# Kernel optimization log

Measured on AMD Instinct MI355X. Metric: run time of the kernel, lower is better.

Reference implementation:

```python
import jax, jax.numpy as jnp
import numpy as np
from jax import lax
import math

POOL = 7
SPATIAL_SCALE = 0.125
SCORE_THRESH = 0.05
NMS_THRESH = 0.5
DET_PER_IMG = 100
NUM_CLASSES = 81
NUM_STAGES = 3
FEAT_CH = 256
CLIP_VAL = math.log(1000.0 / 16)
STDS = ((0.1, 0.1, 0.2, 0.2), (0.05, 0.05, 0.1, 0.1), (0.033, 0.033, 0.067, 0.067))


def setup_inputs() -> dict:
    key = jax.random.key(0)
    ks = jax.random.split(key, 12)
    B, N, img = 2, 512, 512
    features = jax.random.normal(ks[0], (B, FEAT_CH, 64, 64), jnp.float32)
    cx = jax.random.uniform(ks[1], (B, N)) * img
    cy = jax.random.uniform(ks[2], (B, N)) * img
    w = 16.0 + jax.random.uniform(ks[3], (B, N)) * 240.0
    h = 16.0 + jax.random.uniform(ks[4], (B, N)) * 240.0
    proposals = jnp.stack([
        jnp.clip(cx - 0.5 * w, 0.0, img), jnp.clip(cy - 0.5 * h, 0.0, img),
        jnp.clip(cx + 0.5 * w, 0.0, img), jnp.clip(cy + 0.5 * h, 0.0, img)], axis=-1)
    in_dim = FEAT_CH * POOL * POOL
    sc = 0.02
    return {
        'features': features,
        'proposals': proposals,
        'fc1_w': jax.random.normal(ks[5], (NUM_STAGES, in_dim, 1024), jnp.float32) * sc,
        'fc1_b': jnp.zeros((NUM_STAGES, 1024), jnp.float32),
        'fc2_w': jax.random.normal(ks[6], (NUM_STAGES, 1024, 1024), jnp.float32) * sc,
        'fc2_b': jnp.zeros((NUM_STAGES, 1024), jnp.float32),
        'cls_w': jax.random.normal(ks[7], (NUM_STAGES, 1024, NUM_CLASSES), jnp.float32) * sc,
        'cls_b': jnp.zeros((NUM_STAGES, NUM_CLASSES), jnp.float32),
        'bbox_w': jax.random.normal(ks[8], (NUM_STAGES, 1024, 4), jnp.float32) * sc,
        'bbox_b': jnp.zeros((NUM_STAGES, 4), jnp.float32),
        'image_size': 512,
    }


def _bilinear(feat, gx, gy):
    # feat [C,H,W]; gx,gy [N,P,P] float coords
    C, H, W = feat.shape
    x = jnp.clip(gx, 0.0, W - 1.0)
    y = jnp.clip(gy, 0.0, H - 1.0)
    x0f, y0f = jnp.floor(x), jnp.floor(y)
    x0 = x0f.astype(jnp.int32)
    y0 = y0f.astype(jnp.int32)
    x1 = jnp.minimum(x0 + 1, W - 1)
    y1 = jnp.minimum(y0 + 1, H - 1)
    dx = (x - x0f)[None]
    dy = (y - y0f)[None]
    v = (feat[:, y0, x0] * (1 - dy) * (1 - dx) + feat[:, y0, x1] * (1 - dy) * dx
         + feat[:, y1, x0] * dy * (1 - dx) + feat[:, y1, x1] * dy * dx)
    return v  # [C,N,P,P]


def roi_align(feat, boxes):
    # feat [C,H,W], boxes [N,4] in feature-map coords
    x1, y1, x2, y2 = boxes[:, 0], boxes[:, 1], boxes[:, 2], boxes[:, 3]
    bw = jnp.maximum(x2 - x1, 1.0) / POOL
    bh = jnp.maximum(y2 - y1, 1.0) / POOL
    c = jnp.arange(POOL, dtype=boxes.dtype) + 0.5
    xs = x1[:, None] + c * bw[:, None]  # [N,P]
    ys = y1[:, None] + c * bh[:, None]
    N = boxes.shape[0]
    gx = jnp.broadcast_to(xs[:, None, :], (N, POOL, POOL))
    gy = jnp.broadcast_to(ys[:, :, None], (N, POOL, POOL))
    return jnp.transpose(_bilinear(feat, gx, gy), (1, 0, 2, 3))  # [N,C,P,P]


def decode_boxes(proposals, deltas, stds):
    px1, py1, px2, py2 = proposals[:, 0], proposals[:, 1], proposals[:, 2], proposals[:, 3]
    pw = jnp.maximum(px2 - px1, 1e-6)
    ph = jnp.maximum(py2 - py1, 1e-6)
    pcx = px1 + 0.5 * pw
    pcy = py1 + 0.5 * ph
    wx, wy, ww, wh = stds
    dx = deltas[:, 0] * wx
    dy = deltas[:, 1] * wy
    dw = jnp.minimum(deltas[:, 2] * ww, CLIP_VAL)
    dh = jnp.minimum(deltas[:, 3] * wh, CLIP_VAL)
    cx = dx * pw + pcx
    cy = dy * ph + pcy
    w = jnp.exp(dw) * pw
    h = jnp.exp(dh) * ph
    return jnp.stack([cx - 0.5 * w, cy - 0.5 * h, cx + 0.5 * w, cy + 0.5 * h], axis=1)


def clip_boxes(b, img):
    return jnp.stack([jnp.clip(b[:, 0], 0.0, img), jnp.clip(b[:, 1], 0.0, img),
                      jnp.clip(b[:, 2], 0.0, img), jnp.clip(b[:, 3], 0.0, img)], axis=1)


def nms_per_image(boxes, probs, img):
    # boxes [N,4], probs [N,C]
    N, C = probs.shape
    Cm = C - 1  # skip background class 0
    labels = jnp.broadcast_to(jnp.arange(1, C, dtype=jnp.int32), (N, Cm)).reshape(-1)
    b = jnp.broadcast_to(boxes[:, None, :], (N, Cm, 4)).reshape(-1, 4)
    s = probs[:, 1:].reshape(-1)
    ws = b[:, 2] - b[:, 0]
    hs = b[:, 3] - b[:, 1]
    valid = (s > SCORE_THRESH) & (ws >= 1.0) & (hs >= 1.0)
    s = jnp.where(valid, s, -1.0)
    # class-offset trick == batched_nms
    ob = b + (labels.astype(b.dtype) * (img + 2.0))[:, None]
    area = jnp.maximum(ob[:, 2] - ob[:, 0], 0.0) * jnp.maximum(ob[:, 3] - ob[:, 1], 0.0)

    def step(s_live, _):
        i = jnp.argmax(s_live)
        si = s_live[i]
        bi = ob[i]
        ix1 = jnp.maximum(bi[0], ob[:, 0])
        iy1 = jnp.maximum(bi[1], ob[:, 1])
        ix2 = jnp.minimum(bi[2], ob[:, 2])
        iy2 = jnp.minimum(bi[3], ob[:, 3])
        inter = jnp.maximum(ix2 - ix1, 0.0) * jnp.maximum(iy2 - iy1, 0.0)
        iou = inter / (area[i] + area - inter + 1e-9)
        s_live = jnp.where(iou > NMS_THRESH, -1.0, s_live)
        s_live = s_live.at[i].set(-1.0)
        return s_live, (i, si)

    _, (idx, sel_s) = lax.scan(step, s, None, length=DET_PER_IMG)
    flag = sel_s > 0.0
    out_boxes = jnp.where(flag[:, None], b[idx], 0.0)
    out_scores = jnp.where(flag, sel_s, 0.0)
    out_labels = jnp.where(flag, labels[idx], 0)
    return out_boxes, out_scores, out_labels


def reference(features, proposals, fc1_w, fc1_b, fc2_w, fc2_b, cls_w, cls_b, bbox_w, bbox_b, image_size):
    B, Cf, H, W = features.shape
    N = proposals.shape[1]
    img = float(image_size)
    cur = proposals  # [B,N,4]
    logits = None
    for st in range(NUM_STAGES):
        pooled = jax.vmap(lambda f, bx: roi_align(f, bx * SPATIAL_SCALE))(features, cur)  # [B,N,C,P,P]
        x = pooled.reshape(B * N, -1)
        x = jax.nn.relu(x @ fc1_w[st] + fc1_b[st])
        x = jax.nn.relu(x @ fc2_w[st] + fc2_b[st])
        logits = x @ cls_w[st] + cls_b[st]  # [B*N, C]
        deltas = x @ bbox_w[st] + bbox_b[st]  # [B*N, 4]
        dec = clip_boxes(decode_boxes(cur.reshape(-1, 4), deltas, STDS[st]), img)
        cur = dec.reshape(B, N, 4)
    probs = jax.nn.softmax(logits.reshape(B, N, -1), axis=-1)
    boxes, scores, labels = jax.vmap(lambda bb, pp: nms_per_image(bb, pp, img))(cur, probs)
    return boxes, scores, labels
```

## Files before the change

kernel.cpp:

```cpp
#include <hip/hip_runtime.h>
#include <math.h>

#define NPROP 512
#define NB 2
#define NROWS (NB*NPROP)
#define FCH 256
#define FH 64
#define FW 64
#define INDIM (FCH*7*7)
#define HID 1024
#define NCLS 81
#define CAND_PER_IMG (NPROP*(NCLS-1))
#define CLIPV 4.1351666f

typedef _Float16 f16x8 __attribute__((ext_vector_type(8)));
typedef float f32x4 __attribute__((ext_vector_type(4)));
typedef unsigned int u32;
typedef unsigned long long u64;

__device__ __forceinline__ void gload16(const void* g, void* l) {
    __builtin_amdgcn_global_load_lds((const __attribute__((address_space(1))) u32*)g,
                                     (__attribute__((address_space(3))) u32*)l, 16, 0, 0);
}

#define XHI_OFF    0ull
#define XLO_OFF    25690112ull
#define WT1HI_OFF  51380224ull
#define WT1LO_OFF  77070336ull
#define WT2HI_OFF  102760448ull
#define WT2LO_OFF  104857600ull
#define H1HI_OFF   106954752ull
#define H1LO_OFF   109051904ull
#define H2_OFF     111149056ull
#define CWT_OFF    115343360ull
#define BWT_OFF    116338688ull
#define PROBS_OFF  116387840ull
#define CUR_OFF    116719616ull
#define CNT_OFF    116736000ull
#define CCS_OFF    116737024ull
#define CCOB_OFF   117064704ull
#define CCAR_OFF   118375424ull
#define CCBX_OFF   118703104ull
#define CCIX_OFF   120013824ull
#define SVS_OFF    120341504ull
#define SVB_OFF    120423424ull
#define SVI_OFF    120751104ull
#define SVC_OFF    120833024ull
#define PART_OFF   121489408ull

__global__ void init_kernel(int* ccnt) {
    if (threadIdx.x < 160) ccnt[threadIdx.x] = 0;
}

__global__ __launch_bounds__(256) void roi_align_kernel(
    const float* __restrict__ feat, const float* __restrict__ boxes,
    _Float16* __restrict__ Xhi, _Float16* __restrict__ Xlo)
{
    int r = blockIdx.x;
    int b = r >> 9;
    const float* f = feat + (size_t)b * (FCH*FH*FW);
    __shared__ float sb[4];
    __shared__ int   sx0[49], sx1[49], sy0[49], sy1[49];
    __shared__ float sw00[49], sw01[49], sw10[49], sw11[49];
    int tid = threadIdx.x;
    if (tid == 0) {
        float x1 = boxes[r*4+0]*0.125f, y1 = boxes[r*4+1]*0.125f;
        float x2 = boxes[r*4+2]*0.125f, y2 = boxes[r*4+3]*0.125f;
        sb[0] = x1; sb[1] = y1;
        sb[2] = fmaxf(x2-x1, 1.0f) / 7.0f;
        sb[3] = fmaxf(y2-y1, 1.0f) / 7.0f;
    }
    __syncthreads();
    if (tid < 49) {
        int py = tid / 7, px = tid - py*7;
        float gx = sb[0] + ((float)px + 0.5f)*sb[2];
        float gy = sb[1] + ((float)py + 0.5f)*sb[3];
        gx = fminf(fmaxf(gx, 0.0f), 63.0f);
        gy = fminf(fmaxf(gy, 0.0f), 63.0f);
        float x0f = floorf(gx), y0f = floorf(gy);
        int x0 = (int)x0f, y0 = (int)y0f;
        sx0[tid] = x0; sy0[tid] = y0;
        sx1[tid] = min(x0+1, 63); sy1[tid] = min(y0+1, 63);
        float dx = gx - x0f, dy = gy - y0f;
        sw00[tid] = (1.0f-dy)*(1.0f-dx);
        sw01[tid] = (1.0f-dy)*dx;
        sw10[tid] = dy*(1.0f-dx);
        sw11[tid] = dy*dx;
    }
    __syncthreads();
    size_t xbase = (size_t)r * INDIM;
    for (int i = tid; i < INDIM; i += 256) {
        int c = i / 49;
        int p = i - c*49;
        const float* fc = f + c*(FH*FW);
        int r0 = sy0[p]*FW, r1 = sy1[p]*FW;
        float v = fc[r0 + sx0[p]]*sw00[p] + fc[r0 + sx1[p]]*sw01[p]
                + fc[r1 + sx0[p]]*sw10[p] + fc[r1 + sx1[p]]*sw11[p];
        float vs = v * 32.0f;
        _Float16 h = (_Float16)vs;
        Xhi[xbase + i] = h;
        Xlo[xbase + i] = (_Float16)(vs - (float)h);
    }
}

__global__ __launch_bounds__(256) void trans_limb(
    const float* __restrict__ in, _Float16* __restrict__ hi, _Float16* __restrict__ lo,
    int K, int N, float scale)
{
    __shared__ float t[32][33];
    int tx = threadIdx.x & 31, ty = threadIdx.x >> 5;
    int n0 = blockIdx.x << 5, k0 = blockIdx.y << 5;
#pragma unroll
    for (int r = 0; r < 4; ++r)
        t[ty + 8*r][tx] = in[(size_t)(k0 + ty + 8*r)*N + n0 + tx];
    __syncthreads();
#pragma unroll
    for (int r = 0; r < 4; ++r) {
        int n = n0 + ty + 8*r, k = k0 + tx;
        float v = t[tx][ty + 8*r] * scale;
        _Float16 h = (_Float16)v;
        hi[(size_t)n*K + k] = h;
        lo[(size_t)n*K + k] = (_Float16)(v - (float)h);
    }
}

__global__ __launch_bounds__(256) void trans_naive(
    const float* __restrict__ in, float* __restrict__ out, int K, int N, int batch)
{
    int idx = blockIdx.x*256 + threadIdx.x;
    int per = K*N;
    if (idx >= per*batch) return;
    int b = idx / per;
    int rem = idx - b*per;
    int n = rem / K, k = rem - n*K;
    out[idx] = in[(size_t)b*per + (size_t)k*N + n];
}

__global__ __launch_bounds__(512, 2) void mfma_gemm_limb256(
    const _Float16* __restrict__ Ahi, const _Float16* __restrict__ Alo,
    const _Float16* __restrict__ Bhi, const _Float16* __restrict__ Blo,
    float* __restrict__ part, int K, int base, int extra)
{
    extern __shared__ __align__(16) char ldsraw[];
    const int tid = threadIdx.x;
    const int lane = tid & 63;
    const int w = tid >> 6;
    const int wm = w >> 2, wn = w & 3;
    const int kg = lane >> 4, lr = lane & 15;
    const int bid = blockIdx.x;
    const int z = bid & 15;
    const int tile = bid >> 4;
    const int bx = tile & 3, by = tile >> 2;
    const int row0 = by << 8, col0 = bx << 8;
    const int zsteps = base + (z < extra ? 1 : 0);
    const int kb0 = (z*base + (z < extra ? z : extra)) * 32;

    const int sp = w >> 1;
    const int sbase = (w & 1) * 8;
    const _Float16* pl = (sp == 0) ? Ahi : (sp == 1) ? Alo : (sp == 2) ? Bhi : Blo;
    const int rc0 = (sp < 2) ? row0 : col0;
    const _Float16* sG = pl + (size_t)(rc0 + lane)*K + kb0;

    f32x4 acc[8][4];
#pragma unroll
    for (int i = 0; i < 8; ++i)
#pragma unroll
        for (int j = 0; j < 4; ++j) acc[i][j] = (f32x4){0.f, 0.f, 0.f, 0.f};

    auto STAGE = [&](int bufoff, int koff) {
#pragma unroll
        for (int j = 0; j < 8; ++j) {
            int sub = sbase + j;
            int ks = sub >> 2, rblk = sub & 3;
            const void* g = (const void*)(sG + (size_t)(rblk*64)*K + koff + ks*8);
            void* l = (void*)(ldsraw + bufoff + sp*16384 + ks*4096 + rblk*1024);
            gload16(g, l);
        }
    };

    STAGE(0, 0);
    if (zsteps > 1) STAGE(65536, 32);

    for (int t = 0; t < zsteps; ++t) {
        if (t + 1 < zsteps) asm volatile("s_waitcnt vmcnt(8)" ::: "memory");
        else                asm volatile("s_waitcnt vmcnt(0)" ::: "memory");
        __builtin_amdgcn_s_barrier();
        asm volatile("" ::: "memory");
        const char* Lb = ldsraw + ((t & 1) ? 65536 : 0);
        f16x8 Bh[4], Bl[4];
#pragma unroll
        for (int ni = 0; ni < 4; ++ni) {
            int s = (kg*256 + wn*64 + ni*16 + lr) * 16;
            Bh[ni] = *(const f16x8*)(Lb + 2*16384 + s);
            Bl[ni] = *(const f16x8*)(Lb + 3*16384 + s);
        }
#pragma unroll
        for (int mi = 0; mi < 8; ++mi) {
            int s = (kg*256 + wm*128 + mi*16 + lr) * 16;
            f16x8 ah = *(const f16x8*)(Lb + s);
            f16x8 al = *(const f16x8*)(Lb + 16384 + s);
#pragma unroll
            for (int ni = 0; ni < 4; ++ni) {
                acc[mi][ni] = __builtin_amdgcn_mfma_f32_16x16x32_f16(ah, Bh[ni], acc[mi][ni], 0, 0, 0);
                acc[mi][ni] = __builtin_amdgcn_mfma_f32_16x16x32_f16(ah, Bl[ni], acc[mi][ni], 0, 0, 0);
                acc[mi][ni] = __builtin_amdgcn_mfma_f32_16x16x32_f16(al, Bh[ni], acc[mi][ni], 0, 0, 0);
            }
        }
        asm volatile("" ::: "memory");
        __builtin_amdgcn_s_barrier();
        asm volatile("" ::: "memory");
        if (t + 2 < zsteps) STAGE((t & 1) ? 65536 : 0, (t+2)*32);
    }

    float* cb = part + ((size_t)z << 20)
              + (size_t)row0*HID + col0 + wn*64 + lr;
#pragma unroll
    for (int mi = 0; mi < 8; ++mi) {
#pragma unroll
        for (int j = 0; j < 4; ++j) {
            int row = wm*128 + mi*16 + kg*4 + j;
            float* pr = cb + (size_t)row*HID;
            pr[0]  = acc[mi][0][j];
            pr[16] = acc[mi][1][j];
            pr[32] = acc[mi][2][j];
            pr[48] = acc[mi][3][j];
        }
    }
}

__global__ __launch_bounds__(256) void mfma_gemm_limb(
    const _Float16* __restrict__ Ahi, const _Float16* __restrict__ Alo,
    const _Float16* __restrict__ Bhi, const _Float16* __restrict__ Blo,
    float* __restrict__ part, int K, int base, int extra, int lognz)
{
    __shared__ __align__(16) _Float16 lds[2][4][512][8];
    const int tid = threadIdx.x;
    const int lane = tid & 63;
    const int w = tid >> 6, wm = w >> 1, wn = w & 1;
    const int kg = lane >> 4, lr = lane & 15;
    const int bid = blockIdx.x;
    const int nzm = (1 << lognz) - 1;
    const int z = bid & nzm;
    const int bx = (bid >> lognz) & 7;
    const int by = bid >> (lognz + 3);
    const int row0 = by << 7, col0 = bx << 7;
    const int zsteps = base + (z < extra ? 1 : 0);
    const int kb0 = (z*base + (z < extra ? z : extra)) * 32;
    const int r_ = tid & 127;
    const int ks1 = tid >> 7;
    const int wb = tid & 192;

    const _Float16* srcA0 = Ahi + (size_t)(row0 + r_) * K + kb0 + ks1*8;
    const _Float16* srcA1 = Alo + (size_t)(row0 + r_) * K + kb0 + ks1*8;
    const _Float16* srcB0 = Bhi + (size_t)(col0 + r_) * K + kb0 + ks1*8;
    const _Float16* srcB1 = Blo + (size_t)(col0 + r_) * K + kb0 + ks1*8;

    f32x4 acc[4][4];
#pragma unroll
    for (int i = 0; i < 4; ++i)
#pragma unroll
        for (int j = 0; j < 4; ++j) acc[i][j] = (f32x4){0.f, 0.f, 0.f, 0.f};

#define STAGE(bf, off) do { \
    _Float16* Lb = &lds[bf][0][0][0]; \
    gload16(srcA0 + (off),      (void*)(Lb + (0*512 +       wb)*8)); \
    gload16(srcA0 + (off) + 16, (void*)(Lb + (0*512 + 256 + wb)*8)); \
    gload16(srcA1 + (off),      (void*)(Lb + (1*512 +       wb)*8)); \
    gload16(srcA1 + (off) + 16, (void*)(Lb + (1*512 + 256 + wb)*8)); \
    gload16(srcB0 + (off),      (void*)(Lb + (2*512 +       wb)*8)); \
    gload16(srcB0 + (off) + 16, (void*)(Lb + (2*512 + 256 + wb)*8)); \
    gload16(srcB1 + (off),      (void*)(Lb + (3*512 +       wb)*8)); \
    gload16(srcB1 + (off) + 16, (void*)(Lb + (3*512 + 256 + wb)*8)); \
} while (0)

    STAGE(0, 0);
    if (1 < zsteps) STAGE(1, 32);
    for (int t = 0; t < zsteps; ++t) {
        if (t + 1 < zsteps) asm volatile("s_waitcnt vmcnt(8)" ::: "memory");
        else                asm volatile("s_waitcnt vmcnt(0)" ::: "memory");
        __builtin_amdgcn_s_barrier();
        const _Float16* Lr = &lds[t & 1][0][0][0];
        f16x8 Ah[4], Al[4], Bh[4], Bl[4];
#pragma unroll
        for (int mi = 0; mi < 4; ++mi) {
            int s = kg*128 + wm*64 + mi*16 + lr;
            Ah[mi] = *(const f16x8*)(Lr + (0*512 + s)*8);
            Al[mi] = *(const f16x8*)(Lr + (1*512 + s)*8);
        }
#pragma unroll
        for (int ni = 0; ni < 4; ++ni) {
            int s = kg*128 + wn*64 + ni*16 + lr;
            Bh[ni] = *(const f16x8*)(Lr + (2*512 + s)*8);
            Bl[ni] = *(const f16x8*)(Lr + (3*512 + s)*8);
        }
        asm volatile("s_waitcnt lgkmcnt(0)" ::: "memory");
        __builtin_amdgcn_sched_barrier(0);
        __builtin_amdgcn_s_barrier();
        if (t + 2 < zsteps) STAGE(t & 1, (t+2)*32);
#pragma unroll
        for (int mi = 0; mi < 4; ++mi)
#pragma unroll
            for (int ni = 0; ni < 4; ++ni) {
                acc[mi][ni] = __builtin_amdgcn_mfma_f32_16x16x32_f16(Ah[mi], Bh[ni], acc[mi][ni], 0, 0, 0);
                acc[mi][ni] = __builtin_amdgcn_mfma_f32_16x16x32_f16(Ah[mi], Bl[ni], acc[mi][ni], 0, 0, 0);
                acc[mi][ni] = __builtin_amdgcn_mfma_f32_16x16x32_f16(Al[mi], Bh[ni], acc[mi][ni], 0, 0, 0);
            }
    }
#undef STAGE

    float* cb = part + ((size_t)z << 20)
              + (size_t)row0*HID + col0 + wn*64 + lr;
#pragma unroll
    for (int mi = 0; mi < 4; ++mi) {
#pragma unroll
        for (int j = 0; j < 4; ++j) {
            int row = wm*64 + mi*16 + kg*4 + j;
            float* pr = cb + (size_t)row*HID;
            pr[0]  = acc[mi][0][j];
            pr[16] = acc[mi][1][j];
            pr[32] = acc[mi][2][j];
            pr[48] = acc[mi][3][j];
        }
    }
}

__global__ __launch_bounds__(256) void reduce_bias_relu(
    const float* __restrict__ part, const float* __restrict__ bias,
    float* __restrict__ out32, _Float16* __restrict__ outhi, _Float16* __restrict__ outlo,
    int nsplit, int mode)
{
    int gid = blockIdx.x*256 + threadIdx.x;
    float s = 0.f;
    for (int p = 0; p < nsplit; ++p) s += part[((size_t)p << 20) + gid];
    s = s * (1.0f/2048.0f) + bias[gid & (HID-1)];
    s = fmaxf(s, 0.f);
    if (mode == 0) {
        out32[gid] = s;
    } else {
        float vs = s * 32.0f;
        _Float16 h = (_Float16)vs;
        outhi[gid] = h;
        outlo[gid] = (_Float16)(vs - (float)h);
    }
}

__global__ __launch_bounds__(512) void heads_kernel(
    const float* __restrict__ X, const float* __restrict__ cwT, const float* __restrict__ cb,
    const float* __restrict__ bwT, const float* __restrict__ bbb,
    float* __restrict__ cur, float* __restrict__ probs,
    const int* __restrict__ img_sz, int stage, int write_probs)
{
    __shared__ float xs[4][1024];
    __shared__ float lg[4][96];
    int tid = threadIdx.x;
    int lr = tid >> 7;
    int j  = tid & 127;
    int row0 = blockIdx.x * 4;
    for (int i = tid; i < 4096; i += 512)
        xs[i >> 10][i & 1023] = X[(size_t)(row0 + (i >> 10))*1024 + (i & 1023)];
    __syncthreads();
    int row = row0 + lr;
    if (j < 85) {
        const float* wrow = (j < 81) ? (cwT + (size_t)j*HID) : (bwT + (size_t)(j-81)*HID);
        float acc = (j < 81) ? cb[j] : bbb[j-81];
        const float4* w4 = (const float4*)wrow;
#pragma unroll 4
        for (int k4 = 0; k4 < 256; ++k4) {
            float4 wv = w4[k4];
            const float* xr = &xs[lr][k4*4];
            acc = fmaf(xr[0], wv.x, acc);
            acc = fmaf(xr[1], wv.y, acc);
            acc = fmaf(xr[2], wv.z, acc);
            acc = fmaf(xr[3], wv.w, acc);
        }
        lg[lr][j] = acc;
    }
    __syncthreads();
    if (j == 0) {
        float img = (float)(*img_sz);
        float px1 = cur[row*4+0], py1 = cur[row*4+1];
        float px2 = cur[row*4+2], py2 = cur[row*4+3];
        float pw = fmaxf(px2-px1, 1e-6f), ph = fmaxf(py2-py1, 1e-6f);
        float pcx = px1 + 0.5f*pw, pcy = py1 + 0.5f*ph;
        float wx, wy, ww, wh;
        if (stage == 0)      { wx=0.1f;   wy=0.1f;   ww=0.2f;   wh=0.2f;   }
        else if (stage == 1) { wx=0.05f;  wy=0.05f;  ww=0.1f;   wh=0.1f;   }
        else                 { wx=0.033f; wy=0.033f; ww=0.067f; wh=0.067f; }
        float dx = lg[lr][81]*wx, dy = lg[lr][82]*wy;
        float dw = fminf(lg[lr][83]*ww, CLIPV);
        float dh = fminf(lg[lr][84]*wh, CLIPV);
        float cx = dx*pw + pcx, cy = dy*ph + pcy;
        float w = expf(dw)*pw, h = expf(dh)*ph;
        cur[row*4+0] = fminf(fmaxf(cx - 0.5f*w, 0.f), img);
        cur[row*4+1] = fminf(fmaxf(cy - 0.5f*h, 0.f), img);
        cur[row*4+2] = fminf(fmaxf(cx + 0.5f*w, 0.f), img);
        cur[row*4+3] = fminf(fmaxf(cy + 0.5f*h, 0.f), img);
    }
    if (write_probs) {
        if (j == 1) {
            float m = lg[lr][0];
            for (int c2 = 1; c2 < 81; ++c2) m = fmaxf(m, lg[lr][c2]);
            float s = 0.f;
            for (int c2 = 0; c2 < 81; ++c2) s += expf(lg[lr][c2] - m);
            lg[lr][88] = m; lg[lr][89] = s;
        }
        __syncthreads();
        if (j < 81)
            probs[(size_t)row*81 + j] = expf(lg[lr][j] - lg[lr][88]) / lg[lr][89];
    }
}

__global__ __launch_bounds__(256) void compact_class(
    const float* __restrict__ probs, const float* __restrict__ cur,
    const int* __restrict__ img_sz, int* __restrict__ ccnt,
    float* __restrict__ ccs, float4* __restrict__ ccob, float* __restrict__ ccar,
    float4* __restrict__ ccbx, int* __restrict__ ccix)
{
    int gid = blockIdx.x*256 + threadIdx.x;
    if (gid >= NB*CAND_PER_IMG) return;
    int b = gid / CAND_PER_IMG;
    int rem = gid - b*CAND_PER_IMG;
    int n = rem / 80;
    int cm = rem - n*80;
    int label = cm + 1;
    int r = b*NPROP + n;
    float s = probs[(size_t)r*81 + label];
    float b0 = cur[r*4+0], b1 = cur[r*4+1], b2 = cur[r*4+2], b3 = cur[r*4+3];
    if (s > 0.05f && (b2 - b0) >= 1.0f && (b3 - b1) >= 1.0f) {
        int cls = b*80 + cm;
        int pos = atomicAdd(&ccnt[cls], 1);
        int base = cls*512 + pos;
        float img = (float)(*img_sz);
        float t = (float)label * (img + 2.0f);
        float o0 = b0+t, o1 = b1+t, o2 = b2+t, o3 = b3+t;
        ccs[base] = s;
        ccob[base] = make_float4(o0, o1, o2, o3);
        ccar[base] = fmaxf(o2-o0, 0.f) * fmaxf(o3-o1, 0.f);
        ccbx[base] = make_float4(b0, b1, b2, b3);
        ccix[base] = rem;
    }
}

__global__ __launch_bounds__(64) void class_nms(
    const int* __restrict__ ccnt, const float* __restrict__ ccs,
    const float4* __restrict__ ccob, const float* __restrict__ ccar,
    const float4* __restrict__ ccbx, const int* __restrict__ ccix,
    float* __restrict__ svs, float4* __restrict__ svb, int* __restrict__ svi,
    int* __restrict__ svc)
{
    int cls = blockIdx.x;
    int Nc = ccnt[cls];
    int base = cls*512;
    int lane = threadIdx.x;
    __shared__ float sel[5];
    float s[8]; float4 ob[8]; float a[8]; int ix[8];
    int cntl = 0;
    for (int j = lane; j < Nc; j += 64) {
        s[cntl] = ccs[base+j]; ob[cntl] = ccob[base+j];
        a[cntl] = ccar[base+j]; ix[cntl] = ccix[base+j];
        ++cntl;
    }
    int svn = 0;
    int rounds = (Nc < 100) ? Nc : 100;
    for (int it = 0; it < rounds; ++it) {
        float bs = -1.f; int bi = 0x7fffffff;
        for (int q = 0; q < cntl; ++q)
            if (s[q] > bs || (s[q] == bs && ix[q] < bi)) { bs = s[q]; bi = ix[q]; }
        for (int off = 32; off > 0; off >>= 1) {
            float os = __shfl_xor(bs, off);
            int oi = __shfl_xor(bi, off);
            if (os > bs || (os == bs && oi < bi)) { bs = os; bi = oi; }
        }
        if (bs <= 0.f) break;
        for (int q = 0; q < cntl; ++q) {
            if (s[q] == bs && ix[q] == bi) {
                sel[0] = ob[q].x; sel[1] = ob[q].y; sel[2] = ob[q].z; sel[3] = ob[q].w;
                sel[4] = a[q];
                int slot = cls*128 + svn;
                svs[slot] = bs;
                svb[slot] = ccbx[base + lane + q*64];
                svi[slot] = bi;
                s[q] = -1.f;
            }
        }
        __syncthreads();
        float bi0 = sel[0], bi1 = sel[1], bi2 = sel[2], bi3 = sel[3], ai = sel[4];
        for (int q = 0; q < cntl; ++q) {
            if (s[q] > 0.f) {
                float ix1 = fmaxf(bi0, ob[q].x), iy1 = fmaxf(bi1, ob[q].y);
                float ix2 = fminf(bi2, ob[q].z), iy2 = fminf(bi3, ob[q].w);
                float inter = fmaxf(ix2-ix1, 0.f) * fmaxf(iy2-iy1, 0.f);
                float iou = inter / (ai + a[q] - inter + 1e-9f);
                if (iou > 0.5f) s[q] = -1.f;
            }
        }
        ++svn;
        __syncthreads();
    }
    if (lane == 0) svc[cls] = svn;
}

__global__ __launch_bounds__(256) void merge_topk(
    const float* __restrict__ svs, const float4* __restrict__ svb,
    const int* __restrict__ svi, const int* __restrict__ svc,
    float* __restrict__ out)
{
    extern __shared__ char smem[];
    u64* keys = (u64*)smem;
    u32* pay  = (u32*)(smem + 65536);
    __shared__ int off[81];
    __shared__ int n2s;
    int b = blockIdx.x, tid = threadIdx.x;
    if (tid == 0) {
        int run = 0;
        for (int c = 0; c < 80; ++c) { off[c] = run; run += svc[b*80 + c]; }
        off[80] = run;
        int n2 = 256;
        while (n2 < run) n2 <<= 1;
        n2s = n2;
    }
    __syncthreads();
    int Ns = off[80], n2 = n2s;
    for (int c = 0; c < 80; ++c) {
        int n = off[c+1] - off[c];
        int srcb = (b*80 + c)*128;
        for (int k = tid; k < n; k += 256) {
            int src = srcb + k;
            keys[off[c] + k] = ((u64)__float_as_uint(svs[src]) << 32)
                             | (u64)(0xFFFFFFFFu - (u32)svi[src]);
            pay[off[c] + k] = src;
        }
    }
    for (int i = Ns + tid; i < n2; i += 256) { keys[i] = 0; pay[i] = 0; }
    __syncthreads();
    for (int k = 2; k <= n2; k <<= 1) {
        for (int j = k >> 1; j > 0; j >>= 1) {
            for (int i = tid; i < n2; i += 256) {
                int l = i ^ j;
                if (l > i) {
                    u64 a = keys[i], bb = keys[l];
                    bool dir = ((i & k) == 0);
                    if ((a < bb) == dir) {
                        keys[i] = bb; keys[l] = a;
                        u32 p = pay[i]; pay[i] = pay[l]; pay[l] = p;
                    }
                }
            }
            __syncthreads();
        }
    }
    if (tid < 100) {
        u64 kk = keys[tid];
        if (kk != 0) {
            u32 ci = 0xFFFFFFFFu - (u32)(kk & 0xFFFFFFFFull);
            float4 bx = svb[pay[tid]];
            out[b*400 + tid*4 + 0] = bx.x;
            out[b*400 + tid*4 + 1] = bx.y;
            out[b*400 + tid*4 + 2] = bx.z;
            out[b*400 + tid*4 + 3] = bx.w;
            out[800  + b*100 + tid] = __uint_as_float((u32)(kk >> 32));
            out[1000 + b*100 + tid] = (float)((ci % 80) + 1);
        } else {
            out[b*400 + tid*4 + 0] = 0.f; out[b*400 + tid*4 + 1] = 0.f;
            out[b*400 + tid*4 + 2] = 0.f; out[b*400 + tid*4 + 3] = 0.f;
            out[800  + b*100 + tid] = 0.f;
            out[1000 + b*100 + tid] = 0.f;
        }
    }
}

extern "C" void kernel_launch(void* const* d_in, const int* in_sizes, int n_in,
                              void* d_out, int out_size, void* d_ws, size_t ws_size,
                              hipStream_t stream)
{
    const float* features  = (const float*)d_in[0];
    const float* proposals = (const float*)d_in[1];
    const float* fc1_w = (const float*)d_in[2];
    const float* fc1_b = (const float*)d_in[3];
    const float* fc2_w = (const float*)d_in[4];
    const float* fc2_b = (const float*)d_in[5];
    const float* cls_w = (const float*)d_in[6];
    const float* cls_b = (const float*)d_in[7];
    const float* bbox_w = (const float*)d_in[8];
    const float* bbox_b = (const float*)d_in[9];
    const int* img_sz = (const int*)d_in[10];
    float* out = (float*)d_out;
    char* ws = (char*)d_ws;
    _Float16* xhi   = (_Float16*)(ws + XHI_OFF);
    _Float16* xlo   = (_Float16*)(ws + XLO_OFF);
    _Float16* wt1hi = (_Float16*)(ws + WT1HI_OFF);
    _Float16* wt1lo = (_Float16*)(ws + WT1LO_OFF);
    _Float16* wt2hi = (_Float16*)(ws + WT2HI_OFF);
    _Float16* wt2lo = (_Float16*)(ws + WT2LO_OFF);
    _Float16* h1hi  = (_Float16*)(ws + H1HI_OFF);
    _Float16* h1lo  = (_Float16*)(ws + H1LO_OFF);
    float*  h2     = (float*) (ws + H2_OFF);
    float*  cwT    = (float*) (ws + CWT_OFF);
    float*  bwT    = (float*) (ws + BWT_OFF);
    float*  probs  = (float*) (ws + PROBS_OFF);
    float*  cur    = (float*) (ws + CUR_OFF);
    int*    ccnt   = (int*)   (ws + CNT_OFF);
    float*  ccs    = (float*) (ws + CCS_OFF);
    float4* ccob   = (float4*)(ws + CCOB_OFF);
    float*  ccar   = (float*) (ws + CCAR_OFF);
    float4* ccbx   = (float4*)(ws + CCBX_OFF);
    int*    ccix   = (int*)   (ws + CCIX_OFF);
    float*  svs    = (float*) (ws + SVS_OFF);
    float4* svb    = (float4*)(ws + SVB_OFF);
    int*    svi    = (int*)   (ws + SVI_OFF);
    int*    svc    = (int*)   (ws + SVC_OFF);
    float*  part   = (float*) (ws + PART_OFF);

    init_kernel<<<1, 256, 0, stream>>>(ccnt);
    hipMemcpyAsync(cur, proposals, (size_t)NROWS*4*sizeof(float),
                   hipMemcpyDeviceToDevice, stream);
    trans_naive<<<(3*NCLS*HID + 255)/256, 256, 0, stream>>>(cls_w, cwT, HID, NCLS, 3);
    trans_naive<<<(3*4*HID + 255)/256, 256, 0, stream>>>(bbox_w, bwT, HID, 4, 3);

    for (int st = 0; st < 3; ++st) {
        roi_align_kernel<<<NROWS, 256, 0, stream>>>(features, cur, xhi, xlo);
        trans_limb<<<dim3(HID/32, INDIM/32), 256, 0, stream>>>(
            fc1_w + (size_t)st*INDIM*HID, wt1hi, wt1lo, INDIM, HID, 64.0f);
        mfma_gemm_limb256<<<256, 512, 131072, stream>>>(
            xhi, xlo, wt1hi, wt1lo, part, INDIM, 24, 8);
        reduce_bias_relu<<<(NROWS*HID)/256, 256, 0, stream>>>(
            part, fc1_b + st*HID, nullptr, h1hi, h1lo, 16, 1);
        trans_limb<<<dim3(HID/32, HID/32), 256, 0, stream>>>(
            fc2_w + (size_t)st*HID*HID, wt2hi, wt2lo, HID, HID, 64.0f);
        mfma_gemm_limb<<<512, 256, 0, stream>>>(
            h1hi, h1lo, wt2hi, wt2lo, part, HID, 4, 0, 3);
        reduce_bias_relu<<<(NROWS*HID)/256, 256, 0, stream>>>(
            part, fc2_b + st*HID, h2, nullptr, nullptr, 8, 0);
        heads_kernel<<<NROWS/4, 512, 0, stream>>>(
            h2, cwT + (size_t)st*NCLS*HID, cls_b + st*NCLS,
            bwT + (size_t)st*4*HID, bbox_b + st*4,
            cur, probs, img_sz, st, st == 2 ? 1 : 0);
    }
    compact_class<<<(NB*CAND_PER_IMG)/256, 256, 0, stream>>>(
        probs, cur, img_sz, ccnt, ccs, ccob, ccar, ccbx, ccix);
    class_nms<<<160, 64, 0, stream>>>(
        ccnt, ccs, ccob, ccar, ccbx, ccix, svs, svb, svi, svc);
    merge_topk<<<NB, 256, 98304, stream>>>(
        svs, svb, svi, svc, out);
}
```

Before: 775.3 us.

## Store GEMM operands in k-octet-major layout for contiguous LDS staging loads

Changes the fp16 hi/lo operand buffers (ROI features, transposed weights, hidden activations) from row-major [rows][K] to an [K/8][rows][8] layout, so each 16-byte global_load_lds chunk for consecutive rows is contiguous. The GEMM kernels drop the K stride and index by k-octet. The goal is coalesced wide loads instead of loads strided by K per lane. The producers' writes now scatter in 16-byte pieces, which may cost store efficiency in roi_align, trans_limb and reduce.

```diff
diff --git a/kernel.cpp b/kernel.cpp
--- a/kernel.cpp
+++ b/kernel.cpp
@@ -22,6 +22,7 @@
     __builtin_amdgcn_global_load_lds((const __attribute__((address_space(1))) u32*)g,
                                      (__attribute__((address_space(3))) u32*)l, 16, 0, 0);
 }
+
 
 #define XHI_OFF    0ull
 #define XLO_OFF    25690112ull
@@ -88,7 +89,6 @@
         sw11[tid] = dy*dx;
     }
     __syncthreads();
-    size_t xbase = (size_t)r * INDIM;
     for (int i = tid; i < INDIM; i += 256) {
         int c = i / 49;
         int p = i - c*49;
@@ -98,8 +98,9 @@
                 + fc[r1 + sx0[p]]*sw10[p] + fc[r1 + sx1[p]]*sw11[p];
         float vs = v * 32.0f;
         _Float16 h = (_Float16)vs;
-        Xhi[xbase + i] = h;
-        Xlo[xbase + i] = (_Float16)(vs - (float)h);
+        size_t idx = ((size_t)(i >> 3) << 13) + ((size_t)r << 3) + (i & 7);
+        Xhi[idx] = h;
+        Xlo[idx] = (_Float16)(vs - (float)h);
     }
 }
 
@@ -119,8 +120,9 @@
         int n = n0 + ty + 8*r, k = k0 + tx;
         float v = t[tx][ty + 8*r] * scale;
         _Float16 h = (_Float16)v;
-        hi[(size_t)n*K + k] = h;
-        lo[(size_t)n*K + k] = (_Float16)(v - (float)h);
+        size_t idx = ((size_t)(k >> 3)*N << 3) + ((size_t)n << 3) + (k & 7);
+        hi[idx] = h;
+        lo[idx] = (_Float16)(v - (float)h);
     }
 }
 
@@ -139,7 +141,7 @@
 __global__ __launch_bounds__(512, 2) void mfma_gemm_limb256(
     const _Float16* __restrict__ Ahi, const _Float16* __restrict__ Alo,
     const _Float16* __restrict__ Bhi, const _Float16* __restrict__ Blo,
-    float* __restrict__ part, int K, int base, int extra)
+    float* __restrict__ part, int base, int extra)
 {
     extern __shared__ __align__(16) char ldsraw[];
     const int tid = threadIdx.x;
@@ -153,13 +155,13 @@
     const int bx = tile & 3, by = tile >> 2;
     const int row0 = by << 8, col0 = bx << 8;
     const int zsteps = base + (z < extra ? 1 : 0);
-    const int kb0 = (z*base + (z < extra ? z : extra)) * 32;
+    const int o0 = ((z*base + (z < extra ? z : extra)) * 32) >> 3;
 
     const int sp = w >> 1;
     const int sbase = (w & 1) * 8;
     const _Float16* pl = (sp == 0) ? Ahi : (sp == 1) ? Alo : (sp == 2) ? Bhi : Blo;
     const int rc0 = (sp < 2) ? row0 : col0;
-    const _Float16* sG = pl + (size_t)(rc0 + lane)*K + kb0;
+    const _Float16* sG = pl + ((size_t)(rc0 + lane) << 3);
 
     f32x4 acc[8][4];
 #pragma unroll
@@ -167,19 +169,20 @@
 #pragma unroll
         for (int j = 0; j < 4; ++j) acc[i][j] = (f32x4){0.f, 0.f, 0.f, 0.f};
 
-    auto STAGE = [&](int bufoff, int koff) {
+    auto STAGE = [&](int bufoff, int koct) {
 #pragma unroll
         for (int j = 0; j < 8; ++j) {
             int sub = sbase + j;
             int ks = sub >> 2, rblk = sub & 3;
-            const void* g = (const void*)(sG + (size_t)(rblk*64)*K + koff + ks*8);
+            const void* g = (const void*)(sG + ((size_t)(o0 + koct + ks) << 13)
+                                             + ((size_t)rblk << 9));
             void* l = (void*)(ldsraw + bufoff + sp*16384 + ks*4096 + rblk*1024);
             gload16(g, l);
         }
     };
 
     STAGE(0, 0);
-    if (zsteps > 1) STAGE(65536, 32);
+    if (zsteps > 1) STAGE(65536, 4);
 
     for (int t = 0; t < zsteps; ++t) {
         if (t + 1 < zsteps) asm volatile("s_waitcnt vmcnt(8)" ::: "memory");
@@ -209,7 +212,7 @@
         asm volatile("" ::: "memory");
         __builtin_amdgcn_s_barrier();
         asm volatile("" ::: "memory");
-        if (t + 2 < zsteps) STAGE((t & 1) ? 65536 : 0, (t+2)*32);
+        if (t + 2 < zsteps) STAGE((t & 1) ? 65536 : 0, (t+2)*4);
     }
 
     float* cb = part + ((size_t)z << 20)
@@ -231,7 +234,7 @@
 __global__ __launch_bounds__(256) void mfma_gemm_limb(
     const _Float16* __restrict__ Ahi, const _Float16* __restrict__ Alo,
     const _Float16* __restrict__ Bhi, const _Float16* __restrict__ Blo,
-    float* __restrict__ part, int K, int base, int extra, int lognz)
+    float* __restrict__ part, int base, int extra, int lognz)
 {
     __shared__ __align__(16) _Float16 lds[2][4][512][8];
     const int tid = threadIdx.x;
@@ -245,15 +248,15 @@
     const int by = bid >> (lognz + 3);
     const int row0 = by << 7, col0 = bx << 7;
     const int zsteps = base + (z < extra ? 1 : 0);
-    const int kb0 = (z*base + (z < extra ? z : extra)) * 32;
+    const int o0 = ((z*base + (z < extra ? z : extra)) * 32) >> 3;
     const int r_ = tid & 127;
     const int ks1 = tid >> 7;
     const int wb = tid & 192;
 
-    const _Float16* srcA0 = Ahi + (size_t)(row0 + r_) * K + kb0 + ks1*8;
-    const _Float16* srcA1 = Alo + (size_t)(row0 + r_) * K + kb0 + ks1*8;
-    const _Float16* srcB0 = Bhi + (size_t)(col0 + r_) * K + kb0 + ks1*8;
-    const _Float16* srcB1 = Blo + (size_t)(col0 + r_) * K + kb0 + ks1*8;
+    const _Float16* srcA0 = Ahi + ((size_t)(row0 + r_) << 3);
+    const _Float16* srcA1 = Alo + ((size_t)(row0 + r_) << 3);
+    const _Float16* srcB0 = Bhi + ((size_t)(col0 + r_) << 3);
+    const _Float16* srcB1 = Blo + ((size_t)(col0 + r_) << 3);
 
     f32x4 acc[4][4];
 #pragma unroll
@@ -261,20 +264,20 @@
 #pragma unroll
         for (int j = 0; j < 4; ++j) acc[i][j] = (f32x4){0.f, 0.f, 0.f, 0.f};
 
-#define STAGE(bf, off) do { \
+#define STAGE(bf, oct) do { \
     _Float16* Lb = &lds[bf][0][0][0]; \
-    gload16(srcA0 + (off),      (void*)(Lb + (0*512 +       wb)*8)); \
-    gload16(srcA0 + (off) + 16, (void*)(Lb + (0*512 + 256 + wb)*8)); \
-    gload16(srcA1 + (off),      (void*)(Lb + (1*512 +       wb)*8)); \
-    gload16(srcA1 + (off) + 16, (void*)(Lb + (1*512 + 256 + wb)*8)); \
-    gload16(srcB0 + (off),      (void*)(Lb + (2*512 +       wb)*8)); \
-    gload16(srcB0 + (off) + 16, (void*)(Lb + (2*512 + 256 + wb)*8)); \
-    gload16(srcB1 + (off),      (void*)(Lb + (3*512 +       wb)*8)); \
-    gload16(srcB1 + (off) + 16, (void*)(Lb + (3*512 + 256 + wb)*8)); \
+    gload16(srcA0 + ((size_t)(o0+(oct)+ks1  ) << 13), (void*)(Lb + (0*512 +       wb)*8)); \
+    gload16(srcA0 + ((size_t)(o0+(oct)+ks1+2) << 13), (void*)(Lb + (0*512 + 256 + wb)*8)); \
+    gload16(srcA1 + ((size_t)(o0+(oct)+ks1  ) << 13), (void*)(Lb + (1*512 +       wb)*8)); \
+    gload16(srcA1 + ((size_t)(o0+(oct)+ks1+2) << 13), (void*)(Lb + (1*512 + 256 + wb)*8)); \
+    gload16(srcB0 + ((size_t)(o0+(oct)+ks1  ) << 13), (void*)(Lb + (2*512 +       wb)*8)); \
+    gload16(srcB0 + ((size_t)(o0+(oct)+ks1+2) << 13), (void*)(Lb + (2*512 + 256 + wb)*8)); \
+    gload16(srcB1 + ((size_t)(o0+(oct)+ks1  ) << 13), (void*)(Lb + (3*512 +       wb)*8)); \
+    gload16(srcB1 + ((size_t)(o0+(oct)+ks1+2) << 13), (void*)(Lb + (3*512 + 256 + wb)*8)); \
 } while (0)
 
     STAGE(0, 0);
-    if (1 < zsteps) STAGE(1, 32);
+    if (1 < zsteps) STAGE(1, 4);
     for (int t = 0; t < zsteps; ++t) {
         if (t + 1 < zsteps) asm volatile("s_waitcnt vmcnt(8)" ::: "memory");
         else                asm volatile("s_waitcnt vmcnt(0)" ::: "memory");
@@ -296,7 +299,7 @@
         asm volatile("s_waitcnt lgkmcnt(0)" ::: "memory");
         __builtin_amdgcn_sched_barrier(0);
         __builtin_amdgcn_s_barrier();
-        if (t + 2 < zsteps) STAGE(t & 1, (t+2)*32);
+        if (t + 2 < zsteps) STAGE(t & 1, (t+2)*4);
 #pragma unroll
         for (int mi = 0; mi < 4; ++mi)
 #pragma unroll
@@ -339,8 +342,10 @@
     } else {
         float vs = s * 32.0f;
         _Float16 h = (_Float16)vs;
-        outhi[gid] = h;
-        outlo[gid] = (_Float16)(vs - (float)h);
+        int row = gid >> 10, col = gid & 1023;
+        size_t idx = ((size_t)(col >> 3) << 13) + ((size_t)row << 3) + (col & 7);
+        outhi[idx] = h;
+        outlo[idx] = (_Float16)(vs - (float)h);
     }
 }
 
@@ -622,13 +627,13 @@
         trans_limb<<<dim3(HID/32, INDIM/32), 256, 0, stream>>>(
             fc1_w + (size_t)st*INDIM*HID, wt1hi, wt1lo, INDIM, HID, 64.0f);
         mfma_gemm_limb256<<<256, 512, 131072, stream>>>(
-            xhi, xlo, wt1hi, wt1lo, part, INDIM, 24, 8);
+            xhi, xlo, wt1hi, wt1lo, part, 24, 8);
         reduce_bias_relu<<<(NROWS*HID)/256, 256, 0, stream>>>(
             part, fc1_b + st*HID, nullptr, h1hi, h1lo, 16, 1);
         trans_limb<<<dim3(HID/32, HID/32), 256, 0, stream>>>(
             fc2_w + (size_t)st*HID*HID, wt2hi, wt2lo, HID, HID, 64.0f);
         mfma_gemm_limb<<<512, 256, 0, stream>>>(
-            h1hi, h1lo, wt2hi, wt2lo, part, HID, 4, 0, 3);
+            h1hi, h1lo, wt2hi, wt2lo, part, 4, 0, 3);
         reduce_bias_relu<<<(NROWS*HID)/256, 256, 0, stream>>>(
             part, fc2_b + st*HID, h2, nullptr, nullptr, 8, 0);
         heads_kernel<<<NROWS/4, 512, 0, stream>>>(
```

New measurement: 781.2 us. Within noise of the previous version (+0.8%).
